# Performance work log

Hardware: AMD Instinct MI355X
Metric: run time of the kernel (lower is better)

## Reference

```python
import jax, jax.numpy as jnp
import numpy as np

DEPTH, DIM, HEADS, EXP = 6, 768, 12, 4
B, N = 8, 1024
EPS = 1e-5


def setup_inputs() -> dict:
    key = jax.random.key(0)
    ks = jax.random.split(key, 6)
    s = 0.02
    inp = {
        "x": jax.random.normal(ks[0], (B, N, DIM), dtype=jnp.float32),
        "ln1_g": jnp.ones((DEPTH, DIM), jnp.float32),
        "ln1_b": jnp.zeros((DEPTH, DIM), jnp.float32),
        "wqkv": jax.random.normal(ks[1], (DEPTH, DIM, 3 * DIM), jnp.float32) * s,
        "bqkv": jnp.zeros((DEPTH, 3 * DIM), jnp.float32),
        "ln2_g": jnp.ones((DEPTH, DIM), jnp.float32),
        "ln2_b": jnp.zeros((DEPTH, DIM), jnp.float32),
        "w1": jax.random.normal(ks[2], (DEPTH, DIM, EXP * DIM), jnp.float32) * s,
        "b1": jnp.zeros((DEPTH, EXP * DIM), jnp.float32),
        "w2": jax.random.normal(ks[3], (DEPTH, EXP * DIM, DIM), jnp.float32) * s,
        "b2": jnp.zeros((DEPTH, DIM), jnp.float32),
    }
    return inp


def _layernorm(x, g, b):
    mu = jnp.mean(x, axis=-1, keepdims=True)
    var = jnp.mean(jnp.square(x - mu), axis=-1, keepdims=True)
    return (x - mu) * jax.lax.rsqrt(var + EPS) * g + b


def _block(x, p):
    ln1_g, ln1_b, wqkv, bqkv, ln2_g, ln2_b, w1, b1, w2, b2 = p
    # --- attention (pre-norm, residual) ---
    x1 = _layernorm(x, ln1_g, ln1_b)
    qkv = x1 @ wqkv + bqkv  # [b, n, 3*dim]
    q, k, v = jnp.split(qkv, 3, axis=-1)
    dh = DIM // HEADS
    def heads(t):  # b n (h d) -> b h n d
        return t.reshape(B, N, HEADS, dh).transpose(0, 2, 1, 3)
    q, k, v = heads(q), heads(k), heads(v)
    scale = DIM ** (-0.5)  # NB: module scales by full dim, not head dim
    dots = jnp.einsum("bhnd,bhmd->bhnm", q, k) * scale
    attn = jax.nn.softmax(dots, axis=-1)
    out = jnp.einsum("bhnm,bhmd->bhnd", attn, v)
    out = out.transpose(0, 2, 1, 3).reshape(B, N, DIM)
    x = x + out
    # --- feedforward (pre-norm, residual) ---
    x2 = _layernorm(x, ln2_g, ln2_b)
    h = jax.nn.gelu(x2 @ w1 + b1, approximate=False)
    x = x + (h @ w2 + b2)
    return x


def reference(x, ln1_g, ln1_b, wqkv, bqkv, ln2_g, ln2_b, w1, b1, w2, b2):
    params = (ln1_g, ln1_b, wqkv, bqkv, ln2_g, ln2_b, w1, b1, w2, b2)

    def body(carry, p):
        return _block(carry, p), None

    x, _ = jax.lax.scan(body, x, params)
    return x
```

## Files before the change

kernel.cpp:

```cpp
#include <hip/hip_runtime.h>
#include <hip/hip_bf16.h>
#include <math.h>

#define DEPTH 6
#define DIM   768
#define HEADS 12
#define DH    64
#define NCTX  1024
#define BATCH 8
#define ROWS  (BATCH*NCTX)
#define DIM3  (3*DIM)
#define DIMF  (4*DIM)
#define LNEPS 1e-5f

typedef __attribute__((ext_vector_type(8)))  short short8;
typedef __attribute__((ext_vector_type(4)))  float floatx4;
typedef __attribute__((ext_vector_type(16))) float floatx16;
using bf16 = __hip_bfloat16;
typedef unsigned int u32;

static __device__ __forceinline__ bf16 f2bf(float v){ return __float2bfloat16(v); }
static __device__ __forceinline__ float bf2f(unsigned short u){
    union { unsigned int i; float f; } c; c.i = ((unsigned int)u) << 16; return c.f;
}
static __device__ __forceinline__ unsigned short bfu(float v){ return __bfloat16_as_ushort(f2bf(v)); }
static __device__ __forceinline__ u32 pk2(float a, float b){
    return (u32)bfu(a) | ((u32)bfu(b) << 16);
}

static __device__ __forceinline__ void gl_lds16(const void* g, void* l) {
    __builtin_amdgcn_global_load_lds((const __attribute__((address_space(1))) void*)g,
                                     (__attribute__((address_space(3))) void*)l, 16, 0, 0);
}

__global__ void k_transpose_convert(const float* __restrict__ W, bf16* __restrict__ WT,
                                    int K, int N) {
    __shared__ float tile[32][33];
    int l = blockIdx.z;
    const float* Wl = W + (size_t)l * K * N;
    bf16* WTl = WT + (size_t)l * K * N;
    int n0 = blockIdx.x * 32, k0 = blockIdx.y * 32;
    int tx = threadIdx.x, ty = threadIdx.y;
#pragma unroll
    for (int i = 0; i < 4; i++)
        tile[ty + i*8][tx] = Wl[(size_t)(k0 + ty + i*8) * N + n0 + tx];
    __syncthreads();
#pragma unroll
    for (int i = 0; i < 4; i++)
        WTl[(size_t)(n0 + ty + i*8) * K + k0 + tx] = f2bf(tile[tx][ty + i*8]);
}

__global__ __launch_bounds__(256) void k_layernorm(const float* __restrict__ x,
                                                   const float* __restrict__ g,
                                                   const float* __restrict__ b,
                                                   bf16* __restrict__ y) {
    int row  = blockIdx.x * 4 + (threadIdx.x >> 6);
    int lane = threadIdx.x & 63;
    const float4* xr = (const float4*)(x + (size_t)row * DIM);
    float4 v[3];
    float s = 0.f, s2 = 0.f;
#pragma unroll
    for (int i = 0; i < 3; i++) {
        v[i] = xr[lane + i*64];
        s  += v[i].x + v[i].y + v[i].z + v[i].w;
        s2 += v[i].x*v[i].x + v[i].y*v[i].y + v[i].z*v[i].z + v[i].w*v[i].w;
    }
#pragma unroll
    for (int m = 1; m < 64; m <<= 1) { s += __shfl_xor(s, m); s2 += __shfl_xor(s2, m); }
    float mu  = s * (1.f / DIM);
    float var = s2 * (1.f / DIM) - mu * mu;
    float rs  = rsqrtf(var + LNEPS);
    bf16* yr = y + (size_t)row * DIM;
    const float4* g4 = (const float4*)g;
    const float4* b4 = (const float4*)b;
#pragma unroll
    for (int i = 0; i < 3; i++) {
        float4 gg = g4[lane + i*64], bb = b4[lane + i*64];
        float r0 = (v[i].x - mu) * rs * gg.x + bb.x;
        float r1 = (v[i].y - mu) * rs * gg.y + bb.y;
        float r2 = (v[i].z - mu) * rs * gg.z + bb.z;
        float r3 = (v[i].w - mu) * rs * gg.w + bb.w;
        uint2 u; u.x = pk2(r0, r1); u.y = pk2(r2, r3);
        *(uint2*)&yr[4 * (lane + i*64)] = u;
    }
}

template<int MODE, int BM, int BN>
__global__ __launch_bounds__(256, 2) void k_gemm(const bf16* __restrict__ A,
                                                 const bf16* __restrict__ WT,
                                                 const float* __restrict__ bias,
                                                 bf16* __restrict__ outb,
                                                 float* __restrict__ outf,
                                                 int N, int K) {
    constexpr int IF  = BM / 32;
    constexpr int JF  = BN / 32;
    constexpr int LPT = BM / 64 + BN / 64;
    __shared__ __align__(16) bf16 As[3][BM*32];
    __shared__ __align__(16) bf16 Bs[3][BN*32];
    int nt = N / BN;
    int nwg = gridDim.x;
    int fblk = blockIdx.x;
    int swz = (fblk & 7) * (nwg >> 3) + (fblk >> 3);
    int m0 = (swz / nt) * BM, n0 = (swz % nt) * BN;
    int t = threadIdx.x;
    int lane = t & 63, w = t >> 6;
    int wr = (w >> 1) * (BM / 2), wc = (w & 1) * (BN / 2);
    int lr = lane & 15, lg = lane >> 4;

    floatx4 acc[IF][JF] = {};
    int NT = K >> 5;

    auto STAGE = [&](int ks, int buf) {
        int ko = ks << 5;
#pragma unroll
        for (int ac = 0; ac < BM/64; ac++) {
            int c = ac*256 + t;
            int row = c >> 2, col = (c & 3) * 8;
            gl_lds16(A + (size_t)(m0 + row) * K + ko + col, &As[buf][c * 8]);
        }
#pragma unroll
        for (int bc = 0; bc < BN/64; bc++) {
            int c = bc*256 + t;
            int row = c >> 2, col = (c & 3) * 8;
            gl_lds16(WT + (size_t)(n0 + row) * K + ko + col, &Bs[buf][c * 8]);
        }
    };
    auto WAITC = [&]() {
        if constexpr (LPT == 6)      asm volatile("s_waitcnt vmcnt(6)" ::: "memory");
        else if constexpr (LPT == 4) asm volatile("s_waitcnt vmcnt(4)" ::: "memory");
        else                         asm volatile("s_waitcnt vmcnt(3)" ::: "memory");
    };

    STAGE(0, 0);
    STAGE(1, 1);
    WAITC();
    __builtin_amdgcn_s_barrier();

    for (int kb = 0; kb < NT; kb += 3) {
#pragma unroll
        for (int s = 0; s < 3; s++) {
            int ks = kb + s;
            bool pf = (ks + 2) < NT;
            if (pf) STAGE(ks + 2, (s + 2) % 3);
            short8 af[IF], bfr[JF];
#pragma unroll
            for (int i = 0; i < IF; i++) af[i]  = *(const short8*)&As[s][(wr + i*16 + lr)*32 + lg*8];
#pragma unroll
            for (int j = 0; j < JF; j++) bfr[j] = *(const short8*)&Bs[s][(wc + j*16 + lr)*32 + lg*8];
            __builtin_amdgcn_s_setprio(1);
#pragma unroll
            for (int i = 0; i < IF; i++)
#pragma unroll
                for (int j = 0; j < JF; j++)
                    acc[i][j] = __builtin_amdgcn_mfma_f32_16x16x32_bf16(af[i], bfr[j], acc[i][j], 0, 0, 0);
            __builtin_amdgcn_s_setprio(0);
            if (pf) WAITC();
            else    asm volatile("s_waitcnt vmcnt(0)" ::: "memory");
            __builtin_amdgcn_s_barrier();
        }
    }
#pragma unroll
    for (int i = 0; i < IF; i++)
#pragma unroll
        for (int j = 0; j < JF; j++)
#pragma unroll
            for (int r = 0; r < 4; r++) {
                int row = m0 + wr + i*16 + lg*4 + r;
                int col = n0 + wc + j*16 + lr;
                float vv = acc[i][j][r] + bias[col];
                if (MODE == 0) {
                    outb[(size_t)row * N + col] = f2bf(vv);
                } else if (MODE == 1) {
                    float u = 1.5957691216f * (vv + 0.044715f * vv * vv * vv);
                    float gs = 1.f / (1.f + __expf(-u));
                    outb[(size_t)row * N + col] = f2bf(vv * gs);
                } else {
                    outf[(size_t)row * N + col] += vv;
                }
            }
}

static __device__ __forceinline__ int vt_off(int d, int k) {
    int dw = d * 36 + (k >> 1);
    dw ^= (d & 0x38) >> 1;
    return dw * 2 + (k & 1);
}

__global__ __launch_bounds__(256, 3) void k_attn(const bf16* __restrict__ qkv,
                                                 float* __restrict__ x) {
    int f = blockIdx.x;
    int b  = f & 7;
    int rr = f >> 3;
    int h  = rr % 12;
    int qt = rr / 12;
    int t = threadIdx.x, lane = t & 63, w = t >> 6;
    int q = lane & 31, hi = lane >> 5;
    const size_t bn0 = (size_t)b * NCTX;
    const bf16* Qg = qkv + bn0 * DIM3 + h * DH;
    const bf16* Kg = Qg + DIM;
    const bf16* Vg = Qg + 2 * DIM;
    int q0 = qt * 128 + w * 32;

    const float qs = 0.036084391824351615f * 1.4426950408889634f;
    short8 qf[4];
#pragma unroll
    for (int s = 0; s < 4; s++) {
        short8 raw = *(const short8*)&Qg[(size_t)(q0 + q) * DIM3 + s*16 + hi*8];
        short8 o;
#pragma unroll
        for (int e = 0; e < 8; e++)
            o[e] = (short)bfu(bf2f((unsigned short)raw[e]) * qs);
        qf[s] = o;
    }

    __shared__ __align__(16) bf16 KsS[64*64];
    __shared__ __align__(16) bf16 VTs[64*72];
    __shared__ float wbc[4][32];

    u32* ksw = (u32*)KsS;

    int sr[2], sc[2];
#pragma unroll
    for (int it = 0; it < 2; it++) { int c = it*256 + t; sr[it] = c >> 3; sc[it] = (c & 7) * 8; }

    floatx16 pacc[2] = {};
    float mrow = -3e38f, lrow = 0.f;

    uint4 kreg[2], vreg[2];
#pragma unroll
    for (int it = 0; it < 2; it++) {
        kreg[it] = *(const uint4*)&Kg[(size_t)sr[it] * DIM3 + sc[it]];
        vreg[it] = *(const uint4*)&Vg[(size_t)sr[it] * DIM3 + sc[it]];
    }

    for (int kt = 0; kt < 16; kt++) {
        __syncthreads();
#pragma unroll
        for (int it = 0; it < 2; it++) {
            int row = sr[it], u = sc[it] >> 3;
            *(uint4*)(ksw + row*32 + ((u ^ (row & 7)) << 2)) = kreg[it];
            const bf16* vp = (const bf16*)&vreg[it];
#pragma unroll
            for (int e = 0; e < 8; e++) VTs[vt_off(sc[it] + e, row)] = vp[e];
        }
        __syncthreads();
        if (kt + 1 < 16) {
            int kv0 = (kt + 1) * 64;
#pragma unroll
            for (int it = 0; it < 2; it++) {
                kreg[it] = *(const uint4*)&Kg[(size_t)(kv0 + sr[it]) * DIM3 + sc[it]];
                vreg[it] = *(const uint4*)&Vg[(size_t)(kv0 + sr[it]) * DIM3 + sc[it]];
            }
        }

        floatx16 sacc[2] = {};
        __builtin_amdgcn_s_setprio(1);
#pragma unroll
        for (int kb = 0; kb < 2; kb++) {
#pragma unroll
            for (int s = 0; s < 4; s++) {
                int row = kb*32 + q;
                short8 kf = *(const short8*)(ksw + row*32 + (((2*s + hi) ^ (row & 7)) << 2));
                sacc[kb] = __builtin_amdgcn_mfma_f32_32x32x16_bf16(kf, qf[s], sacc[kb], 0, 0, 0);
            }
        }
        __builtin_amdgcn_s_setprio(0);

        float mx = sacc[0][0];
#pragma unroll
        for (int r = 1; r < 16; r++) mx = fmaxf(mx, sacc[0][r]);
#pragma unroll
        for (int r = 0; r < 16; r++) mx = fmaxf(mx, sacc[1][r]);
        mx = fmaxf(mx, __shfl_xor(mx, 32));
        bool chg = mx > mrow + 8.f;
        if (__any(chg)) {
            float mnew = chg ? mx : mrow;
            float corr = exp2f(mrow - mnew);
            mrow = mnew;
            lrow *= corr;
            wbc[w][q] = corr;
#pragma unroll
            for (int r = 0; r < 16; r++) {
                float c = wbc[w][(r & 3) + 8*(r >> 2) + 4*hi];
                pacc[0][r] *= c; pacc[1][r] *= c;
            }
        }

        float sum = 0.f;
#pragma unroll
        for (int kb = 0; kb < 2; kb++) {
            float pf[16];
#pragma unroll
            for (int r = 0; r < 16; r++) { pf[r] = exp2f(sacc[kb][r] - mrow); sum += pf[r]; }
#pragma unroll
            for (int g = 0; g < 2; g++) {
                u32 a0 = pk2(pf[8*g+0], pf[8*g+1]);
                u32 a1 = pk2(pf[8*g+2], pf[8*g+3]);
                u32 b0 = pk2(pf[8*g+4], pf[8*g+5]);
                u32 b1 = pk2(pf[8*g+6], pf[8*g+7]);
                asm volatile("v_permlane32_swap_b32 %0, %1" : "+v"(a0), "+v"(b0));
                asm volatile("v_permlane32_swap_b32 %0, %1" : "+v"(a1), "+v"(b1));
                union { u32 u[4]; short8 s8; } pa;
                pa.u[0] = a0; pa.u[1] = a1; pa.u[2] = b0; pa.u[3] = b1;
                int ks = 2*kb + g;
                __builtin_amdgcn_s_setprio(1);
#pragma unroll
                for (int db = 0; db < 2; db++) {
                    short8 vb = *(const short8*)&VTs[vt_off(db*32 + q, 16*ks + 8*hi)];
                    pacc[db] = __builtin_amdgcn_mfma_f32_32x32x16_bf16(pa.s8, vb, pacc[db], 0, 0, 0);
                }
                __builtin_amdgcn_s_setprio(0);
            }
        }
        sum += __shfl_xor(sum, 32);
        lrow += sum;
    }

    wbc[w][q] = 1.f / lrow;
    float* xr = x + bn0 * DIM + (size_t)h * DH;
#pragma unroll
    for (int r = 0; r < 16; r++) {
        int qrow = (r & 3) + 8*(r >> 2) + 4*hi;
        float li = wbc[w][qrow];
#pragma unroll
        for (int db = 0; db < 2; db++) {
            int col = db*32 + q;
            xr[(size_t)(q0 + qrow) * DIM + col] += pacc[db][r] * li;
        }
    }
}

extern "C" void kernel_launch(void* const* d_in, const int* in_sizes, int n_in,
                              void* d_out, int out_size, void* d_ws, size_t ws_size,
                              hipStream_t stream) {
    const float* x_in  = (const float*)d_in[0];
    const float* ln1_g = (const float*)d_in[1];
    const float* ln1_b = (const float*)d_in[2];
    const float* wqkv  = (const float*)d_in[3];
    const float* bqkv  = (const float*)d_in[4];
    const float* ln2_g = (const float*)d_in[5];
    const float* ln2_b = (const float*)d_in[6];
    const float* w1    = (const float*)d_in[7];
    const float* b1    = (const float*)d_in[8];
    const float* w2    = (const float*)d_in[9];
    const float* b2    = (const float*)d_in[10];
    float* x = (float*)d_out;

    char* ws = (char*)d_ws;
    size_t off = 0;
    auto alloc = [&](size_t bytes) { void* p = ws + off; off += (bytes + 255) & ~255ull; return p; };
    bf16* wqkvT = (bf16*)alloc((size_t)DEPTH * DIM * DIM3 * 2);
    bf16* w1T   = (bf16*)alloc((size_t)DEPTH * DIM * DIMF * 2);
    bf16* w2T   = (bf16*)alloc((size_t)DEPTH * DIMF * DIM * 2);
    bf16* xn    = (bf16*)alloc((size_t)ROWS * DIM * 2);
    bf16* qkvh  = (bf16*)alloc((size_t)ROWS * DIMF * 2);
    if (off > ws_size) return;

    hipMemcpyAsync(x, x_in, (size_t)ROWS * DIM * 4, hipMemcpyDeviceToDevice, stream);

    k_transpose_convert<<<dim3(DIM3/32, DIM/32,  DEPTH), dim3(32, 8), 0, stream>>>(wqkv, wqkvT, DIM,  DIM3);
    k_transpose_convert<<<dim3(DIMF/32, DIM/32,  DEPTH), dim3(32, 8), 0, stream>>>(w1,   w1T,   DIM,  DIMF);
    k_transpose_convert<<<dim3(DIM/32,  DIMF/32, DEPTH), dim3(32, 8), 0, stream>>>(w2,   w2T,   DIMF, DIM);

    for (int l = 0; l < DEPTH; l++) {
        k_layernorm<<<ROWS/4, 256, 0, stream>>>(x, ln1_g + l*DIM, ln1_b + l*DIM, xn);
        k_gemm<0,256,128><<<dim3((DIM3/128)*(ROWS/256)), 256, 0, stream>>>(
            xn, wqkvT + (size_t)l*DIM*DIM3, bqkv + (size_t)l*DIM3, qkvh, nullptr, DIM3, DIM);
        k_attn<<<dim3(768), 256, 0, stream>>>(qkvh, x);
        k_layernorm<<<ROWS/4, 256, 0, stream>>>(x, ln2_g + l*DIM, ln2_b + l*DIM, xn);
        k_gemm<1,256,128><<<dim3((DIMF/128)*(ROWS/256)), 256, 0, stream>>>(
            xn, w1T + (size_t)l*DIM*DIMF, b1 + (size_t)l*DIMF, qkvh, nullptr, DIMF, DIM);
        k_gemm<2,128,64><<<dim3((DIM/64)*(ROWS/128)), 256, 0, stream>>>(
            qkvh, w2T + (size_t)l*DIMF*DIM, b2 + (size_t)l*DIM, nullptr, x, DIM, DIMF);
    }
}
```

Baseline: 1.619 ms.

## Swizzle GEMM LDS tiles and double attention KV tile to 128 rows

The GEMM kernel now XOR-swizzles the 16-byte column chunks in its LDS A/B tiles, both on the global-to-LDS copy and on the fragment reads, to cut LDS bank conflicts. The attention kernel stages 128 keys/values per iteration instead of 64 and processes them as two 64-row halves. This halves the number of syncthreads barriers and global-load rounds per head tile. The cost is twice the LDS footprint and more prefetch registers, which may lower occupancy at the declared launch bounds.

```diff
diff --git a/kernel.cpp b/kernel.cpp
--- a/kernel.cpp
+++ b/kernel.cpp
@@ -106,6 +106,7 @@
     int lane = t & 63, w = t >> 6;
     int wr = (w >> 1) * (BM / 2), wc = (w & 1) * (BN / 2);
     int lr = lane & 15, lg = lane >> 4;
+    int fcol = (lg ^ ((lane >> 1) & 3)) * 8;
 
     floatx4 acc[IF][JF] = {};
     int NT = K >> 5;
@@ -115,13 +116,13 @@
 #pragma unroll
         for (int ac = 0; ac < BM/64; ac++) {
             int c = ac*256 + t;
-            int row = c >> 2, col = (c & 3) * 8;
+            int row = c >> 2, col = ((c & 3) ^ ((c >> 3) & 3)) * 8;
             gl_lds16(A + (size_t)(m0 + row) * K + ko + col, &As[buf][c * 8]);
         }
 #pragma unroll
         for (int bc = 0; bc < BN/64; bc++) {
             int c = bc*256 + t;
-            int row = c >> 2, col = (c & 3) * 8;
+            int row = c >> 2, col = ((c & 3) ^ ((c >> 3) & 3)) * 8;
             gl_lds16(WT + (size_t)(n0 + row) * K + ko + col, &Bs[buf][c * 8]);
         }
     };
@@ -144,9 +145,9 @@
             if (pf) STAGE(ks + 2, (s + 2) % 3);
             short8 af[IF], bfr[JF];
 #pragma unroll
-            for (int i = 0; i < IF; i++) af[i]  = *(const short8*)&As[s][(wr + i*16 + lr)*32 + lg*8];
-#pragma unroll
-            for (int j = 0; j < JF; j++) bfr[j] = *(const short8*)&Bs[s][(wc + j*16 + lr)*32 + lg*8];
+            for (int i = 0; i < IF; i++) af[i]  = *(const short8*)&As[s][(wr + i*16 + lr)*32 + fcol];
+#pragma unroll
+            for (int j = 0; j < JF; j++) bfr[j] = *(const short8*)&Bs[s][(wc + j*16 + lr)*32 + fcol];
             __builtin_amdgcn_s_setprio(1);
 #pragma unroll
             for (int i = 0; i < IF; i++)
@@ -181,7 +182,7 @@
 }
 
 static __device__ __forceinline__ int vt_off(int d, int k) {
-    int dw = d * 36 + (k >> 1);
+    int dw = d * 72 + (k >> 1);
     dw ^= (d & 0x38) >> 1;
     return dw * 2 + (k & 1);
 }
@@ -213,30 +214,30 @@
         qf[s] = o;
     }
 
-    __shared__ __align__(16) bf16 KsS[64*64];
-    __shared__ __align__(16) bf16 VTs[64*72];
+    __shared__ __align__(16) bf16 KsS[128*64];
+    __shared__ __align__(16) bf16 VTs[64*144];
     __shared__ float wbc[4][32];
 
     u32* ksw = (u32*)KsS;
 
-    int sr[2], sc[2];
-#pragma unroll
-    for (int it = 0; it < 2; it++) { int c = it*256 + t; sr[it] = c >> 3; sc[it] = (c & 7) * 8; }
+    int sr[4], sc[4];
+#pragma unroll
+    for (int it = 0; it < 4; it++) { int c = it*256 + t; sr[it] = c >> 3; sc[it] = (c & 7) * 8; }
 
     floatx16 pacc[2] = {};
     float mrow = -3e38f, lrow = 0.f;
 
-    uint4 kreg[2], vreg[2];
-#pragma unroll
-    for (int it = 0; it < 2; it++) {
+    uint4 kreg[4], vreg[4];
+#pragma unroll
+    for (int it = 0; it < 4; it++) {
         kreg[it] = *(const uint4*)&Kg[(size_t)sr[it] * DIM3 + sc[it]];
         vreg[it] = *(const uint4*)&Vg[(size_t)sr[it] * DIM3 + sc[it]];
     }
 
-    for (int kt = 0; kt < 16; kt++) {
+    for (int kt = 0; kt < 8; kt++) {
         __syncthreads();
 #pragma unroll
-        for (int it = 0; it < 2; it++) {
+        for (int it = 0; it < 4; it++) {
             int row = sr[it], u = sc[it] >> 3;
             *(uint4*)(ksw + row*32 + ((u ^ (row & 7)) << 2)) = kreg[it];
             const bf16* vp = (const bf16*)&vreg[it];
@@ -244,76 +245,81 @@
             for (int e = 0; e < 8; e++) VTs[vt_off(sc[it] + e, row)] = vp[e];
         }
         __syncthreads();
-        if (kt + 1 < 16) {
-            int kv0 = (kt + 1) * 64;
-#pragma unroll
-            for (int it = 0; it < 2; it++) {
+        if (kt + 1 < 8) {
+            int kv0 = (kt + 1) * 128;
+#pragma unroll
+            for (int it = 0; it < 4; it++) {
                 kreg[it] = *(const uint4*)&Kg[(size_t)(kv0 + sr[it]) * DIM3 + sc[it]];
                 vreg[it] = *(const uint4*)&Vg[(size_t)(kv0 + sr[it]) * DIM3 + sc[it]];
             }
         }
 
-        floatx16 sacc[2] = {};
-        __builtin_amdgcn_s_setprio(1);
-#pragma unroll
-        for (int kb = 0; kb < 2; kb++) {
-#pragma unroll
-            for (int s = 0; s < 4; s++) {
-                int row = kb*32 + q;
-                short8 kf = *(const short8*)(ksw + row*32 + (((2*s + hi) ^ (row & 7)) << 2));
-                sacc[kb] = __builtin_amdgcn_mfma_f32_32x32x16_bf16(kf, qf[s], sacc[kb], 0, 0, 0);
-            }
-        }
-        __builtin_amdgcn_s_setprio(0);
-
-        float mx = sacc[0][0];
-#pragma unroll
-        for (int r = 1; r < 16; r++) mx = fmaxf(mx, sacc[0][r]);
-#pragma unroll
-        for (int r = 0; r < 16; r++) mx = fmaxf(mx, sacc[1][r]);
-        mx = fmaxf(mx, __shfl_xor(mx, 32));
-        bool chg = mx > mrow + 8.f;
-        if (__any(chg)) {
-            float mnew = chg ? mx : mrow;
-            float corr = exp2f(mrow - mnew);
-            mrow = mnew;
-            lrow *= corr;
-            wbc[w][q] = corr;
-#pragma unroll
-            for (int r = 0; r < 16; r++) {
-                float c = wbc[w][(r & 3) + 8*(r >> 2) + 4*hi];
-                pacc[0][r] *= c; pacc[1][r] *= c;
-            }
-        }
-
-        float sum = 0.f;
-#pragma unroll
-        for (int kb = 0; kb < 2; kb++) {
-            float pf[16];
-#pragma unroll
-            for (int r = 0; r < 16; r++) { pf[r] = exp2f(sacc[kb][r] - mrow); sum += pf[r]; }
-#pragma unroll
-            for (int g = 0; g < 2; g++) {
-                u32 a0 = pk2(pf[8*g+0], pf[8*g+1]);
-                u32 a1 = pk2(pf[8*g+2], pf[8*g+3]);
-                u32 b0 = pk2(pf[8*g+4], pf[8*g+5]);
-                u32 b1 = pk2(pf[8*g+6], pf[8*g+7]);
-                asm volatile("v_permlane32_swap_b32 %0, %1" : "+v"(a0), "+v"(b0));
-                asm volatile("v_permlane32_swap_b32 %0, %1" : "+v"(a1), "+v"(b1));
-                union { u32 u[4]; short8 s8; } pa;
-                pa.u[0] = a0; pa.u[1] = a1; pa.u[2] = b0; pa.u[3] = b1;
-                int ks = 2*kb + g;
-                __builtin_amdgcn_s_setprio(1);
-#pragma unroll
-                for (int db = 0; db < 2; db++) {
-                    short8 vb = *(const short8*)&VTs[vt_off(db*32 + q, 16*ks + 8*hi)];
-                    pacc[db] = __builtin_amdgcn_mfma_f32_32x32x16_bf16(pa.s8, vb, pacc[db], 0, 0, 0);
+#pragma unroll
+        for (int half = 0; half < 2; half++) {
+            int rbase = half * 64;
+
+            floatx16 sacc[2] = {};
+            __builtin_amdgcn_s_setprio(1);
+#pragma unroll
+            for (int kb = 0; kb < 2; kb++) {
+#pragma unroll
+                for (int s = 0; s < 4; s++) {
+                    int row = rbase + kb*32 + q;
+                    short8 kf = *(const short8*)(ksw + row*32 + (((2*s + hi) ^ (row & 7)) << 2));
+                    sacc[kb] = __builtin_amdgcn_mfma_f32_32x32x16_bf16(kf, qf[s], sacc[kb], 0, 0, 0);
                 }
-                __builtin_amdgcn_s_setprio(0);
-            }
-        }
-        sum += __shfl_xor(sum, 32);
-        lrow += sum;
+            }
+            __builtin_amdgcn_s_setprio(0);
+
+            float mx = sacc[0][0];
+#pragma unroll
+            for (int r = 1; r < 16; r++) mx = fmaxf(mx, sacc[0][r]);
+#pragma unroll
+            for (int r = 0; r < 16; r++) mx = fmaxf(mx, sacc[1][r]);
+            mx = fmaxf(mx, __shfl_xor(mx, 32));
+            bool chg = mx > mrow + 8.f;
+            if (__any(chg)) {
+                float mnew = chg ? mx : mrow;
+                float corr = exp2f(mrow - mnew);
+                mrow = mnew;
+                lrow *= corr;
+                wbc[w][q] = corr;
+#pragma unroll
+                for (int r = 0; r < 16; r++) {
+                    float c = wbc[w][(r & 3) + 8*(r >> 2) + 4*hi];
+                    pacc[0][r] *= c; pacc[1][r] *= c;
+                }
+            }
+
+            float sum = 0.f;
+#pragma unroll
+            for (int kb = 0; kb < 2; kb++) {
+                float pfv[16];
+#pragma unroll
+                for (int r = 0; r < 16; r++) { pfv[r] = exp2f(sacc[kb][r] - mrow); sum += pfv[r]; }
+#pragma unroll
+                for (int g = 0; g < 2; g++) {
+                    u32 a0 = pk2(pfv[8*g+0], pfv[8*g+1]);
+                    u32 a1 = pk2(pfv[8*g+2], pfv[8*g+3]);
+                    u32 b0 = pk2(pfv[8*g+4], pfv[8*g+5]);
+                    u32 b1 = pk2(pfv[8*g+6], pfv[8*g+7]);
+                    asm volatile("v_permlane32_swap_b32 %0, %1" : "+v"(a0), "+v"(b0));
+                    asm volatile("v_permlane32_swap_b32 %0, %1" : "+v"(a1), "+v"(b1));
+                    union { u32 u[4]; short8 s8; } pa;
+                    pa.u[0] = a0; pa.u[1] = a1; pa.u[2] = b0; pa.u[3] = b1;
+                    int kloc = rbase + 16*(2*kb + g) + 8*hi;
+                    __builtin_amdgcn_s_setprio(1);
+#pragma unroll
+                    for (int db = 0; db < 2; db++) {
+                        short8 vb = *(const short8*)&VTs[vt_off(db*32 + q, kloc)];
+                        pacc[db] = __builtin_amdgcn_mfma_f32_32x32x16_bf16(pa.s8, vb, pacc[db], 0, 0, 0);
+                    }
+                    __builtin_amdgcn_s_setprio(0);
+                }
+            }
+            sum += __shfl_xor(sum, 32);
+            lrow += sum;
+        }
     }
 
     wbc[w][q] = 1.f / lrow;
```

New measurement: 1.768 ms. +9.2%, slower.
